# Kernel tuning notes

Hardware: AMD Instinct MI355X
Metric: run time of the kernel (lower is better)

Reference implementation:

```python
import jax, jax.numpy as jnp
import numpy as np

EPS = 1e-7  # tf.keras.backend.epsilon()
NUM_HEADS = 8


def setup_inputs() -> dict:
    key = jax.random.key(0)
    ks = jax.random.split(key, 7)
    B, H, W, C = 4, 128, 128, 512
    glorot = (2.0 / (C + C)) ** 0.5
    x = jax.random.normal(ks[0], (B, H, W, C), dtype=jnp.float32)
    wq = jax.random.normal(ks[1], (C, C), dtype=jnp.float32) * glorot
    bq = jnp.zeros((C,), dtype=jnp.float32)
    wk = jax.random.normal(ks[2], (C, C), dtype=jnp.float32) * glorot
    bk = jnp.zeros((C,), dtype=jnp.float32)
    wv = jax.random.normal(ks[3], (C, C), dtype=jnp.float32) * glorot
    bv = jnp.zeros((C,), dtype=jnp.float32)
    return {"x": x, "wq": wq, "bq": bq, "wk": wk, "bk": bk, "wv": wv, "bv": bv}


def _axial_attention(query, key, value, num_heads):
    B, H, W, C = value.shape
    d = query.shape[-1] // num_heads
    q5 = query.reshape(B, H, W, num_heads, d)
    k5 = key.reshape(B, H, W, num_heads, d)
    # column (vertical) attention: scores over H, per column w -> [B, nh, W, H, H]
    v_att = jnp.einsum("bhwnd,bgwnd->bnwhg", q5, k5)
    # row (horizontal) attention: scores over W, per row h -> [B, nh, H, W, W]
    u_att = jnp.einsum("bhwnd,bhvnd->bnhwv", q5, k5)
    # faithful clip-before-softmax chain from the original module
    v_att = jnp.clip(v_att, -1.0 + EPS, 1.0 - EPS)
    u_att = jnp.clip(u_att, -1.0 + EPS, 1.0 - EPS)
    scale = jnp.sqrt(jnp.asarray(d, dtype=v_att.dtype))
    v_att = v_att / scale
    u_att = u_att / scale
    # safed_softmax: softmax in fp32 (inputs already fp32 here)
    v_att = jax.nn.softmax(v_att.astype(jnp.float32), axis=-1).astype(query.dtype)
    u_att = jax.nn.softmax(u_att.astype(jnp.float32), axis=-1).astype(query.dtype)
    v_att = jnp.where(jnp.isnan(v_att), EPS, v_att)
    u_att = jnp.where(jnp.isnan(u_att), EPS, u_att)
    v_att = jnp.clip(v_att, EPS, 1.0 - EPS)
    u_att = jnp.clip(u_att, EPS, 1.0 - EPS)
    # value: [B, nh, W, H, d]
    val5 = value.reshape(B, H, W, num_heads, d)
    xv = jnp.einsum("bnwhg,bnwgd->bnhwd", v_att, val5.transpose(0, 3, 2, 1, 4))
    xu = jnp.einsum("bnhwv,bnhvd->bnhwd", u_att, xv)
    # transpose (0,2,3,4,1): head index becomes last -> channels ordered [d, nh]
    out = xu.transpose(0, 2, 3, 4, 1).reshape(B, H, W, d * num_heads)
    return out


def reference(x, wq, bq, wk, bk, wv, bv):
    # 1x1 convs == per-pixel dense projections
    query = jnp.einsum("bhwc,cf->bhwf", x, wq) + bq
    key = jnp.einsum("bhwc,cf->bhwf", x, wk) + bk
    value = jnp.einsum("bhwc,cf->bhwf", x, wv) + bv
    return _axial_attention(query, key, value, NUM_HEADS)
```

## Files before the change

kernel.cpp:

```cpp
#include <hip/hip_runtime.h>

typedef unsigned short ush;
typedef __attribute__((ext_vector_type(8))) __bf16 bf16x8;
typedef __attribute__((ext_vector_type(4))) float f32x4;

#define NE 33554432L

__device__ __forceinline__ float b2f(ush u) {
  return __uint_as_float(((unsigned int)u) << 16);
}
__device__ __forceinline__ ush f2b(float f) {
  unsigned int x = __float_as_uint(f);
  x += 0x7fffu + ((x >> 16) & 1u);
  return (ush)(x >> 16);
}
__device__ __forceinline__ bf16x8 bc8(int4 v) { return __builtin_bit_cast(bf16x8, v); }

__device__ __forceinline__ void gload16(const ush* g, ush* l) {
  __builtin_amdgcn_global_load_lds(
      (const __attribute__((address_space(1))) void*)g,
      (__attribute__((address_space(3))) void*)l, 16, 0, 0);
}

__global__ __launch_bounds__(256)
void detect_dtype(const ush* __restrict__ x, int* __restrict__ flag) {
  __shared__ int red[256];
  const int t = threadIdx.x;
  int cnt = 0;
  for (int i = t; i < 16384; i += 256) {
    const int e = (x[i] >> 7) & 0xFF;
    cnt += (e == 0 || (e >= 100 && e <= 142)) ? 1 : 0;
  }
  red[t] = cnt;
  __syncthreads();
  for (int s = 128; s > 0; s >>= 1) {
    if (t < s) red[t] += red[t + s];
    __syncthreads();
  }
  if (t == 0) flag[0] = (red[0] >= 13107) ? 1 : 0;
}

__global__ __launch_bounds__(256)
void pack_x(const void* __restrict__ xin, ush* __restrict__ xb,
            const int* __restrict__ flag) {
  const long i0 = ((long)blockIdx.x * 256 + threadIdx.x) * 8;
  if (*flag) {
    *(int4*)&xb[i0] = *(const int4*)&((const ush*)xin)[i0];
  } else {
    const float* xf = (const float*)xin;
    const float4 a = *(const float4*)&xf[i0];
    const float4 b = *(const float4*)&xf[i0 + 4];
    union { ush u[8]; int4 v; } r;
    r.u[0] = f2b(a.x); r.u[1] = f2b(a.y); r.u[2] = f2b(a.z); r.u[3] = f2b(a.w);
    r.u[4] = f2b(b.x); r.u[5] = f2b(b.y); r.u[6] = f2b(b.z); r.u[7] = f2b(b.w);
    *(int4*)&xb[i0] = r.v;
  }
}

__global__ __launch_bounds__(256)
void pack_w(const void* __restrict__ w0, const void* __restrict__ w1,
            const void* __restrict__ w2, ush* __restrict__ wTb,
            const int* __restrict__ flag) {
  __shared__ ush tile[32][33];
  const void* w = (blockIdx.z == 0) ? w0 : ((blockIdx.z == 1) ? w1 : w2);
  ush* wT = wTb + (long)blockIdx.z * 262144;
  const int bx = blockIdx.x * 32, by = blockIdx.y * 32;
  const int tx = threadIdx.x & 31, ty = threadIdx.x >> 5;
  const int f = *flag;
#pragma unroll
  for (int j = 0; j < 32; j += 8) {
    const int k = by + ty + j, n = bx + tx;
    tile[ty + j][tx] = f ? ((const ush*)w)[k * 512 + n]
                         : f2b(((const float*)w)[k * 512 + n]);
  }
  __syncthreads();
#pragma unroll
  for (int j = 0; j < 32; j += 8)
    wT[(bx + ty + j) * 512 + by + tx] = tile[tx][ty + j];
}

__global__ void pack_bias(const void* __restrict__ b0, const void* __restrict__ b1,
                          const void* __restrict__ b2, float* __restrict__ biasf,
                          const int* __restrict__ flag) {
  const void* b = (blockIdx.x == 0) ? b0 : ((blockIdx.x == 1) ? b1 : b2);
  const int n = threadIdx.x;
  const float v = (*flag) ? b2f(((const ush*)b)[n]) : ((const float*)b)[n];
  biasf[blockIdx.x * 512 + n] = v;
}

__global__ __launch_bounds__(256)
void proj_gemm(const ush* __restrict__ xb, const ush* __restrict__ wTb,
               const float* __restrict__ biasf, ush* __restrict__ qkv) {
  __shared__ ush As[2][4096];
  __shared__ ush Bs[2][4096];

  const int lin = blockIdx.x + (blockIdx.y << 2) + (blockIdx.z << 11);
  const int swz = ((lin & 7) * 768) + (lin >> 3);
  const int z   = swz >> 11;
  const int rem = swz & 2047;
  const int by  = rem >> 2, bx = rem & 3;

  const ush* wt = wTb + (long)z * 262144;
  const float* bias = biasf + z * 512;
  ush* out = qkv + (long)z * NE;

  const int t = threadIdx.x;
  const int lane = t & 63;
  const int wvid = t >> 6;
  const int wm = wvid & 1, wn = wvid >> 1;
  const int col = lane & 15, quad = lane >> 4;

  const long m0 = (long)by * 128;
  const int n0 = bx * 128;

  const int r_in_g = lane >> 2;
  const int swzk = (((lane & 3) ^ ((r_in_g >> 1) & 3)) * 8);
  const int g0 = wvid * 2, g1 = g0 + 1;
  const ush* gA0 = xb + (m0 + g0 * 16 + r_in_g) * 512 + swzk;
  const ush* gA1 = xb + (m0 + g1 * 16 + r_in_g) * 512 + swzk;
  const ush* gB0 = wt + (long)(n0 + g0 * 16 + r_in_g) * 512 + swzk;
  const ush* gB1 = wt + (long)(n0 + g1 * 16 + r_in_g) * 512 + swzk;

  const int kswz = ((quad ^ ((col >> 1) & 3)) * 8);
  int aofs[4], bofs4[4];
#pragma unroll
  for (int i = 0; i < 4; i++) aofs[i] = (wm * 64 + i * 16 + col) * 32 + kswz;
#pragma unroll
  for (int j = 0; j < 4; j++) bofs4[j] = (wn * 64 + j * 16 + col) * 32 + kswz;

  const f32x4 z4 = {0.f, 0.f, 0.f, 0.f};
  f32x4 acc[4][4];
#pragma unroll
  for (int i = 0; i < 4; i++)
#pragma unroll
    for (int j = 0; j < 4; j++) acc[i][j] = z4;

  gload16(gA0, &As[0][g0 * 512]);
  gload16(gA1, &As[0][g1 * 512]);
  gload16(gB0, &Bs[0][g0 * 512]);
  gload16(gB1, &Bs[0][g1 * 512]);
  __syncthreads();

  int cur = 0;
  for (int k0 = 0; k0 < 512; k0 += 32) {
    const int nk = k0 + 32;
    if (nk < 512) {
      const int nb = cur ^ 1;
      gload16(gA0 + nk, &As[nb][g0 * 512]);
      gload16(gA1 + nk, &As[nb][g1 * 512]);
      gload16(gB0 + nk, &Bs[nb][g0 * 512]);
      gload16(gB1 + nk, &Bs[nb][g1 * 512]);
    }
    bf16x8 a[4], b[4];
#pragma unroll
    for (int i = 0; i < 4; i++) a[i] = bc8(*(const int4*)&As[cur][aofs[i]]);
#pragma unroll
    for (int j = 0; j < 4; j++) b[j] = bc8(*(const int4*)&Bs[cur][bofs4[j]]);
#pragma unroll
    for (int i = 0; i < 4; i++)
#pragma unroll
      for (int j = 0; j < 4; j++)
        acc[i][j] = __builtin_amdgcn_mfma_f32_16x16x32_bf16(a[i], b[j], acc[i][j], 0, 0, 0);
    __syncthreads();
    cur ^= 1;
  }

#pragma unroll
  for (int j = 0; j < 4; j++) {
    const int n = n0 + wn * 64 + j * 16 + col;
    const float bb = bias[n];
#pragma unroll
    for (int i = 0; i < 4; i++) {
      const long row0 = m0 + wm * 64 + i * 16 + quad * 4;
#pragma unroll
      for (int r = 0; r < 4; r++)
        out[(row0 + r) * 512 + n] = f2b(acc[i][j][r] + bb);
    }
  }
}

#define QS_STRIDE 72
#define VT_STRIDE 136
#define P_STRIDE  136
#define OS_STRIDE 72

__device__ __forceinline__ int vt_idx(int d, int g) {
  return d * VT_STRIDE + ((((g >> 3) ^ ((d >> 3) & 7)) << 3) | (g & 7));
}

template<int PASS>
__global__ __launch_bounds__(512, 4)
void axial_attn_mfma(const ush* __restrict__ Qb, const ush* __restrict__ Kb,
                     ush* __restrict__ Vb, float* __restrict__ xuf,
                     const int bofs) {
  __shared__ ush smem[27136];
  ush* Qs = smem;
  ush* Ks = smem + 9216;
  ush* Vt = smem + 18432;
  ush* P  = smem;

  const int b = blockIdx.z + bofs, n = blockIdx.y, pp = blockIdx.x;
  long base; int stride;
  if (PASS == 1) { base = ((long)b * 16384 + pp) * 512 + n * 64; stride = 65536; }
  else           { base = ((long)(b * 128 + pp) * 128) * 512 + n * 64; stride = 512; }

  const int t = threadIdx.x;
#pragma unroll
  for (int it = 0; it < 2; it++) {
    const int c = t + it * 512;
    const int row = c >> 3, c8 = c & 7;
    const long g = base + (long)row * stride + c8 * 8;
    int4 q = *(const int4*)(Qb + g);
    int4 k = *(const int4*)(Kb + g);
    int4 v = *(const int4*)(Vb + g);
    *(int4*)&Qs[row * QS_STRIDE + c8 * 8] = q;
    *(int4*)&Ks[row * QS_STRIDE + c8 * 8] = k;
    union { int4 i4; ush u[8]; } vu; vu.i4 = v;
#pragma unroll
    for (int dd = 0; dd < 8; dd++)
      Vt[vt_idx(c8 * 8 + dd, row)] = vu.u[dd];
  }
  __syncthreads();

  const int lane = t & 63, wv = t >> 6;
  const int col = lane & 15, quad = lane >> 4;
  const int m0 = wv * 16;
  const f32x4 z4 = {0.f, 0.f, 0.f, 0.f};

  f32x4 sacc[8];
#pragma unroll
  for (int j = 0; j < 8; j++) sacc[j] = z4;
  __builtin_amdgcn_s_setprio(1);
#pragma unroll
  for (int k0 = 0; k0 < 64; k0 += 32) {
    bf16x8 a, kb[8];
    a = bc8(*(const int4*)&Qs[(m0 + col) * QS_STRIDE + k0 + quad * 8]);
#pragma unroll
    for (int j = 0; j < 8; j++)
      kb[j] = bc8(*(const int4*)&Ks[(j * 16 + col) * QS_STRIDE + k0 + quad * 8]);
#pragma unroll
    for (int j = 0; j < 8; j++)
      sacc[j] = __builtin_amdgcn_mfma_f32_16x16x32_bf16(a, kb[j], sacc[j], 0, 0, 0);
  }
  __builtin_amdgcn_s_setprio(0);

  const float CLIP = 1.0f - 1e-7f;
  float e[8][4], inv[4];
#pragma unroll
  for (int r = 0; r < 4; r++) {
    float part = 0.f;
#pragma unroll
    for (int j = 0; j < 8; j++) {
      float s = sacc[j][r];
      s = fminf(fmaxf(s, -CLIP), CLIP) * 0.125f;
      const float ee = __expf(s);
      e[j][r] = ee;
      part += ee;
    }
    part += __shfl_xor(part, 1);
    part += __shfl_xor(part, 2);
    part += __shfl_xor(part, 4);
    part += __shfl_xor(part, 8);
    inv[r] = 1.0f / part;
  }
  __syncthreads();

#pragma unroll
  for (int r = 0; r < 4; r++) {
    const int row = m0 + quad * 4 + r;
#pragma unroll
    for (int j = 0; j < 8; j++) {
      const float pv = fminf(fmaxf(e[j][r] * inv[r], 1e-7f), CLIP);
      P[row * P_STRIDE + j * 16 + col] = f2b(pv);
    }
  }
  __syncthreads();

  f32x4 oacc[4];
#pragma unroll
  for (int j = 0; j < 4; j++) oacc[j] = z4;
  __builtin_amdgcn_s_setprio(1);
#pragma unroll
  for (int k0 = 0; k0 < 128; k0 += 32) {
    bf16x8 a, vb[4];
    a = bc8(*(const int4*)&P[(m0 + col) * P_STRIDE + k0 + quad * 8]);
#pragma unroll
    for (int j = 0; j < 4; j++)
      vb[j] = bc8(*(const int4*)&Vt[vt_idx(j * 16 + col, k0 + quad * 8)]);
#pragma unroll
    for (int j = 0; j < 4; j++)
      oacc[j] = __builtin_amdgcn_mfma_f32_16x16x32_bf16(a, vb[j], oacc[j], 0, 0, 0);
  }
  __builtin_amdgcn_s_setprio(0);

  if (PASS == 1) {
    __syncthreads();
    ush* Os = smem;
#pragma unroll
    for (int r = 0; r < 4; r++) {
      const int row = m0 + quad * 4 + r;
#pragma unroll
      for (int j = 0; j < 4; j++)
        Os[row * OS_STRIDE + j * 16 + col] = f2b(oacc[j][r]);
    }
    __syncthreads();
#pragma unroll
    for (int it = 0; it < 2; it++) {
      const int g2 = t + it * 512;
      const int row = g2 >> 3, c8 = g2 & 7;
      *(int4*)&Vb[base + (long)row * stride + c8 * 8] =
          *(const int4*)&Os[row * OS_STRIDE + c8 * 8];
    }
  } else {
    const long xbase = (((long)(blockIdx.z * 8 + n) * 128 + pp) * 128) * 64;
#pragma unroll
    for (int r = 0; r < 4; r++) {
      const int row = m0 + quad * 4 + r;
#pragma unroll
      for (int j = 0; j < 4; j++)
        xuf[xbase + (long)row * 64 + j * 16 + col] = oacc[j][r];
    }
  }
}

__global__ __launch_bounds__(256)
void out_interleave(const float* __restrict__ xu, void* __restrict__ outp,
                    const int* __restrict__ flagp, const int bofs) {
  __shared__ float lds[8192];
  const int bz = blockIdx.z, h = blockIdx.y, w0 = blockIdx.x * 16;
  const int t = threadIdx.x;
#pragma unroll
  for (int n = 0; n < 8; n++) {
    const float* src = xu + ((((long)(bz * 8 + n)) * 128 + h) * 128 + w0) * 64;
    const int e = t * 4, w = e >> 6, d = e & 63;
    const float4 v = *(const float4*)&src[e];
    const int dr = (d + n * 8) & 63;
    *(float4*)&lds[(n * 16 + w) * 64 + dr] = v;
  }
  __syncthreads();
  const int flg = *flagp;
  const long obase = (((long)(bz + bofs) * 128 + h) * 128 + w0) * 512;
  const int tc = t & 127, c0 = tc * 4;
  const int d = c0 >> 3, n0 = c0 & 7;
#pragma unroll
  for (int ro = 0; ro < 8; ro++) {
    const int w = (t >> 7) * 8 + ro;
    float r[4];
#pragma unroll
    for (int k = 0; k < 4; k++) {
      const int n = n0 + k;
      r[k] = lds[(n * 16 + w) * 64 + ((d + n * 8) & 63)];
    }
    const long oi = obase + (long)w * 512 + c0;
    if (flg) {
      union { ush u[4]; int2 v; } o;
      o.u[0] = f2b(r[0]); o.u[1] = f2b(r[1]);
      o.u[2] = f2b(r[2]); o.u[3] = f2b(r[3]);
      *(int2*)&((ush*)outp)[oi] = o.v;
    } else {
      float4 o; o.x = r[0]; o.y = r[1]; o.z = r[2]; o.w = r[3];
      *(float4*)&((float*)outp)[oi] = o;
    }
  }
}

extern "C" void kernel_launch(void* const* d_in, const int* in_sizes, int n_in,
                              void* d_out, int out_size, void* d_ws, size_t ws_size,
                              hipStream_t stream) {
  const void* x  = d_in[0];
  const void* wq = d_in[1];
  const void* bq = d_in[2];
  const void* wk = d_in[3];
  const void* bk = d_in[4];
  const void* wv = d_in[5];
  const void* bv = d_in[6];

  char* ws = (char*)d_ws;
  int*   flag  = (int*)ws;
  float* biasf = (float*)(ws + 256);
  ush*   wTb   = (ush*)(ws + 8192);
  ush*   xb    = (ush*)(ws + 8192 + 1572864);
  float* xuf   = (float*)(ws + 8192 + 1572864);
  ush*   qkv   = (ush*)(ws + 8192 + 1572864 + 67108864);

  dim3 blk(256);
  detect_dtype<<<1, blk, 0, stream>>>((const ush*)x, flag);
  pack_bias<<<3, 512, 0, stream>>>(bq, bk, bv, biasf, flag);
  pack_w<<<dim3(16, 16, 3), blk, 0, stream>>>(wq, wk, wv, wTb, flag);
  pack_x<<<16384, blk, 0, stream>>>(x, xb, flag);

  ush* Q = qkv;
  ush* K = Q + NE;
  ush* V = K + NE;
  proj_gemm<<<dim3(4, 512, 3), blk, 0, stream>>>(xb, wTb, biasf, Q);
  axial_attn_mfma<1><<<dim3(128, 8, 4), dim3(512), 0, stream>>>(Q, K, V, nullptr, 0);
  for (int half = 0; half < 2; half++) {
    axial_attn_mfma<2><<<dim3(128, 8, 2), dim3(512), 0, stream>>>(Q, K, V, xuf, half * 2);
    out_interleave<<<dim3(8, 128, 2), blk, 0, stream>>>(xuf, d_out, flag, half * 2);
  }
}
```

Baseline: 546.7 us.

## Loop attention blocks over multiple heads with register-prefetched next-head loads

Each attention block now handles several heads in sequence instead of one: all 8 heads in pass 1, 4 heads in pass 2. The Q/K/V tiles for the next head are loaded into registers while the current head's MFMA and softmax run. This hides global load latency and amortizes block launch and setup. In exchange there are fewer blocks (512 per pass instead of 4096/2048), which lowers parallelism and tail utilization, and pass 1 uses more LDS because a separate output staging buffer is added.

Result: no change. 550.4 us (+0.7%).

```diff
diff --git a/kernel.cpp b/kernel.cpp
--- a/kernel.cpp
+++ b/kernel.cpp
@@ -193,134 +193,149 @@
 void axial_attn_mfma(const ush* __restrict__ Qb, const ush* __restrict__ Kb,
                      ush* __restrict__ Vb, float* __restrict__ xuf,
                      const int bofs) {
-  __shared__ ush smem[27136];
+  __shared__ ush smem[(PASS == 1) ? 36352 : 27136];
   ush* Qs = smem;
   ush* Ks = smem + 9216;
   ush* Vt = smem + 18432;
   ush* P  = smem;
-
-  const int b = blockIdx.z + bofs, n = blockIdx.y, pp = blockIdx.x;
-  long base; int stride;
-  if (PASS == 1) { base = ((long)b * 16384 + pp) * 512 + n * 64; stride = 65536; }
-  else           { base = ((long)(b * 128 + pp) * 128) * 512 + n * 64; stride = 512; }
+  ush* Os = smem + 27136;
+
+  const int pp = blockIdx.x;
+  const int NH = (PASS == 1) ? 8 : 4;
+  const int b = blockIdx.y + ((PASS == 1) ? 0 : bofs);
+  const int nstart = (PASS == 1) ? 0 : (blockIdx.z * 4);
+
+  long base0; int stride;
+  if (PASS == 1) { base0 = ((long)b * 16384 + pp) * 512; stride = 65536; }
+  else           { base0 = ((long)(b * 128 + pp) * 128) * 512; stride = 512; }
 
   const int t = threadIdx.x;
-#pragma unroll
-  for (int it = 0; it < 2; it++) {
-    const int c = t + it * 512;
-    const int row = c >> 3, c8 = c & 7;
-    const long g = base + (long)row * stride + c8 * 8;
-    int4 q = *(const int4*)(Qb + g);
-    int4 k = *(const int4*)(Kb + g);
-    int4 v = *(const int4*)(Vb + g);
-    *(int4*)&Qs[row * QS_STRIDE + c8 * 8] = q;
-    *(int4*)&Ks[row * QS_STRIDE + c8 * 8] = k;
-    union { int4 i4; ush u[8]; } vu; vu.i4 = v;
-#pragma unroll
-    for (int dd = 0; dd < 8; dd++)
-      Vt[vt_idx(c8 * 8 + dd, row)] = vu.u[dd];
-  }
-  __syncthreads();
+  const int srow0 = t >> 3, c8 = t & 7;
+  const long o0 = base0 + (long)srow0 * stride + c8 * 8;
+  const long o1 = base0 + (long)(srow0 + 64) * stride + c8 * 8;
 
   const int lane = t & 63, wv = t >> 6;
   const int col = lane & 15, quad = lane >> 4;
   const int m0 = wv * 16;
   const f32x4 z4 = {0.f, 0.f, 0.f, 0.f};
-
-  f32x4 sacc[8];
-#pragma unroll
-  for (int j = 0; j < 8; j++) sacc[j] = z4;
-  __builtin_amdgcn_s_setprio(1);
-#pragma unroll
-  for (int k0 = 0; k0 < 64; k0 += 32) {
-    bf16x8 a, kb[8];
-    a = bc8(*(const int4*)&Qs[(m0 + col) * QS_STRIDE + k0 + quad * 8]);
-#pragma unroll
-    for (int j = 0; j < 8; j++)
-      kb[j] = bc8(*(const int4*)&Ks[(j * 16 + col) * QS_STRIDE + k0 + quad * 8]);
-#pragma unroll
-    for (int j = 0; j < 8; j++)
-      sacc[j] = __builtin_amdgcn_mfma_f32_16x16x32_bf16(a, kb[j], sacc[j], 0, 0, 0);
-  }
-  __builtin_amdgcn_s_setprio(0);
-
   const float CLIP = 1.0f - 1e-7f;
-  float e[8][4], inv[4];
-#pragma unroll
-  for (int r = 0; r < 4; r++) {
-    float part = 0.f;
-#pragma unroll
-    for (int j = 0; j < 8; j++) {
-      float s = sacc[j][r];
-      s = fminf(fmaxf(s, -CLIP), CLIP) * 0.125f;
-      const float ee = __expf(s);
-      e[j][r] = ee;
-      part += ee;
-    }
-    part += __shfl_xor(part, 1);
-    part += __shfl_xor(part, 2);
-    part += __shfl_xor(part, 4);
-    part += __shfl_xor(part, 8);
-    inv[r] = 1.0f / part;
-  }
-  __syncthreads();
-
-#pragma unroll
-  for (int r = 0; r < 4; r++) {
-    const int row = m0 + quad * 4 + r;
-#pragma unroll
-    for (int j = 0; j < 8; j++) {
-      const float pv = fminf(fmaxf(e[j][r] * inv[r], 1e-7f), CLIP);
-      P[row * P_STRIDE + j * 16 + col] = f2b(pv);
-    }
-  }
-  __syncthreads();
-
-  f32x4 oacc[4];
-#pragma unroll
-  for (int j = 0; j < 4; j++) oacc[j] = z4;
-  __builtin_amdgcn_s_setprio(1);
-#pragma unroll
-  for (int k0 = 0; k0 < 128; k0 += 32) {
-    bf16x8 a, vb[4];
-    a = bc8(*(const int4*)&P[(m0 + col) * P_STRIDE + k0 + quad * 8]);
-#pragma unroll
-    for (int j = 0; j < 4; j++)
-      vb[j] = bc8(*(const int4*)&Vt[vt_idx(j * 16 + col, k0 + quad * 8)]);
-#pragma unroll
-    for (int j = 0; j < 4; j++)
-      oacc[j] = __builtin_amdgcn_mfma_f32_16x16x32_bf16(a, vb[j], oacc[j], 0, 0, 0);
-  }
-  __builtin_amdgcn_s_setprio(0);
-
-  if (PASS == 1) {
-    __syncthreads();
-    ush* Os = smem;
+
+  int4 qr0, qr1, kr0, kr1, vr0, vr1;
+#define LOADH(nn_) do { const long nn = (long)(nn_) * 64;          \
+    qr0 = *(const int4*)(Qb + o0 + nn); qr1 = *(const int4*)(Qb + o1 + nn); \
+    kr0 = *(const int4*)(Kb + o0 + nn); kr1 = *(const int4*)(Kb + o1 + nn); \
+    vr0 = *(const int4*)(Vb + o0 + nn); vr1 = *(const int4*)(Vb + o1 + nn); \
+  } while (0)
+
+  LOADH(nstart);
+
+  for (int hn = 0; hn < NH; ++hn) {
+    const int n = nstart + hn;
+    *(int4*)&Qs[srow0 * QS_STRIDE + c8 * 8] = qr0;
+    *(int4*)&Qs[(srow0 + 64) * QS_STRIDE + c8 * 8] = qr1;
+    *(int4*)&Ks[srow0 * QS_STRIDE + c8 * 8] = kr0;
+    *(int4*)&Ks[(srow0 + 64) * QS_STRIDE + c8 * 8] = kr1;
+    {
+      union { int4 i4; ush u[8]; } vu;
+      vu.i4 = vr0;
+#pragma unroll
+      for (int dd = 0; dd < 8; dd++) Vt[vt_idx(c8 * 8 + dd, srow0)] = vu.u[dd];
+      vu.i4 = vr1;
+#pragma unroll
+      for (int dd = 0; dd < 8; dd++) Vt[vt_idx(c8 * 8 + dd, srow0 + 64)] = vu.u[dd];
+    }
+    __syncthreads();
+    if (hn + 1 < NH) LOADH(n + 1);
+
+    f32x4 sacc[8];
+#pragma unroll
+    for (int j = 0; j < 8; j++) sacc[j] = z4;
+    __builtin_amdgcn_s_setprio(1);
+#pragma unroll
+    for (int k0 = 0; k0 < 64; k0 += 32) {
+      bf16x8 a, kb[8];
+      a = bc8(*(const int4*)&Qs[(m0 + col) * QS_STRIDE + k0 + quad * 8]);
+#pragma unroll
+      for (int j = 0; j < 8; j++)
+        kb[j] = bc8(*(const int4*)&Ks[(j * 16 + col) * QS_STRIDE + k0 + quad * 8]);
+#pragma unroll
+      for (int j = 0; j < 8; j++)
+        sacc[j] = __builtin_amdgcn_mfma_f32_16x16x32_bf16(a, kb[j], sacc[j], 0, 0, 0);
+    }
+    __builtin_amdgcn_s_setprio(0);
+
+    float e[8][4], inv[4];
+#pragma unroll
+    for (int r = 0; r < 4; r++) {
+      float part = 0.f;
+#pragma unroll
+      for (int j = 0; j < 8; j++) {
+        float s = sacc[j][r];
+        s = fminf(fmaxf(s, -CLIP), CLIP) * 0.125f;
+        const float ee = __expf(s);
+        e[j][r] = ee;
+        part += ee;
+      }
+      part += __shfl_xor(part, 1);
+      part += __shfl_xor(part, 2);
+      part += __shfl_xor(part, 4);
+      part += __shfl_xor(part, 8);
+      inv[r] = 1.0f / part;
+    }
+    __syncthreads();
+
 #pragma unroll
     for (int r = 0; r < 4; r++) {
       const int row = m0 + quad * 4 + r;
 #pragma unroll
+      for (int j = 0; j < 8; j++) {
+        const float pv = fminf(fmaxf(e[j][r] * inv[r], 1e-7f), CLIP);
+        P[row * P_STRIDE + j * 16 + col] = f2b(pv);
+      }
+    }
+    __syncthreads();
+
+    f32x4 oacc[4];
+#pragma unroll
+    for (int j = 0; j < 4; j++) oacc[j] = z4;
+    __builtin_amdgcn_s_setprio(1);
+#pragma unroll
+    for (int k0 = 0; k0 < 128; k0 += 32) {
+      bf16x8 a, vb[4];
+      a = bc8(*(const int4*)&P[(m0 + col) * P_STRIDE + k0 + quad * 8]);
+#pragma unroll
       for (int j = 0; j < 4; j++)
-        Os[row * OS_STRIDE + j * 16 + col] = f2b(oacc[j][r]);
-    }
-    __syncthreads();
-#pragma unroll
-    for (int it = 0; it < 2; it++) {
-      const int g2 = t + it * 512;
-      const int row = g2 >> 3, c8 = g2 & 7;
-      *(int4*)&Vb[base + (long)row * stride + c8 * 8] =
-          *(const int4*)&Os[row * OS_STRIDE + c8 * 8];
-    }
-  } else {
-    const long xbase = (((long)(blockIdx.z * 8 + n) * 128 + pp) * 128) * 64;
-#pragma unroll
-    for (int r = 0; r < 4; r++) {
-      const int row = m0 + quad * 4 + r;
+        vb[j] = bc8(*(const int4*)&Vt[vt_idx(j * 16 + col, k0 + quad * 8)]);
 #pragma unroll
       for (int j = 0; j < 4; j++)
-        xuf[xbase + (long)row * 64 + j * 16 + col] = oacc[j][r];
-    }
-  }
+        oacc[j] = __builtin_amdgcn_mfma_f32_16x16x32_bf16(a, vb[j], oacc[j], 0, 0, 0);
+    }
+    __builtin_amdgcn_s_setprio(0);
+    __syncthreads();
+
+    if (PASS == 1) {
+#pragma unroll
+      for (int r = 0; r < 4; r++) {
+        const int row = m0 + quad * 4 + r;
+#pragma unroll
+        for (int j = 0; j < 4; j++)
+          Os[row * OS_STRIDE + j * 16 + col] = f2b(oacc[j][r]);
+      }
+      __syncthreads();
+      *(int4*)&Vb[o0 + (long)n * 64] = *(const int4*)&Os[srow0 * OS_STRIDE + c8 * 8];
+      *(int4*)&Vb[o1 + (long)n * 64] = *(const int4*)&Os[(srow0 + 64) * OS_STRIDE + c8 * 8];
+    } else {
+      const long xbase = (((long)(blockIdx.y * 8 + n) * 128 + pp) * 128) * 64;
+#pragma unroll
+      for (int r = 0; r < 4; r++) {
+        const int row = m0 + quad * 4 + r;
+#pragma unroll
+        for (int j = 0; j < 4; j++)
+          xuf[xbase + (long)row * 64 + j * 16 + col] = oacc[j][r];
+      }
+    }
+  }
+#undef LOADH
 }
 
 __global__ __launch_bounds__(256)
@@ -393,9 +408,9 @@
   ush* K = Q + NE;
   ush* V = K + NE;
   proj_gemm<<<dim3(4, 512, 3), blk, 0, stream>>>(xb, wTb, biasf, Q);
-  axial_attn_mfma<1><<<dim3(128, 8, 4), dim3(512), 0, stream>>>(Q, K, V, nullptr, 0);
+  axial_attn_mfma<1><<<dim3(128, 4), dim3(512), 0, stream>>>(Q, K, V, nullptr, 0);
   for (int half = 0; half < 2; half++) {
-    axial_attn_mfma<2><<<dim3(128, 8, 2), dim3(512), 0, stream>>>(Q, K, V, xuf, half * 2);
+    axial_attn_mfma<2><<<dim3(128, 2, 2), dim3(512), 0, stream>>>(Q, K, V, xuf, half * 2);
     out_interleave<<<dim3(8, 128, 2), blk, 0, stream>>>(xuf, d_out, flag, half * 2);
   }
 }
```
